# Performance work log

Hardware: AMD Instinct MI355X
Metric: run time of the kernel (lower is better)

Reference implementation:

```python
import jax, jax.numpy as jnp
import numpy as np

S, N, H = 2048, 32, 1024   # source len, batch, hidden_size
E = 1024                   # input_size (attention MLP width)


def setup_inputs() -> dict:
    key = jax.random.key(0)
    ks = jax.random.split(key, 8)
    sc_h = 1.0 / np.sqrt(H)
    sc_e = 1.0 / np.sqrt(E)
    return {
        "out_e": jax.random.normal(ks[0], (S, N, H), dtype=jnp.float32),
        "hidden_d": jax.random.normal(ks[1], (1, N, H), dtype=jnp.float32),
        "W1": jax.random.uniform(ks[2], (E, H), jnp.float32, -sc_h, sc_h),
        "b1": jax.random.uniform(ks[3], (E,), jnp.float32, -sc_h, sc_h),
        "W2": jax.random.uniform(ks[4], (E, H), jnp.float32, -sc_h, sc_h),
        "b2": jax.random.uniform(ks[5], (E,), jnp.float32, -sc_h, sc_h),
        "W3": jax.random.uniform(ks[6], (1, E), jnp.float32, -sc_e, sc_e),
        "b3": jax.random.uniform(ks[7], (1,), jnp.float32, -sc_e, sc_e),
    }


def reference(out_e, hidden_d, W1, b1, W2, b2, W3, b3):
    # hidden_d (1,N,H) broadcasts against out_e (S,N,H); no explicit repeat needed.
    h1 = jnp.einsum('one,he->onh'.replace('e', 'x'), hidden_d, W1.T) if False else None
    # linear1(hidden_d): (1,N,E); linear2(out_e): (S,N,E)
    proj = jnp.tanh(hidden_d @ W1.T + b1 + out_e @ W2.T + b2)      # (S,N,E)
    a = proj @ W3.T + b3                                           # (S,N,1)
    alpha = jax.nn.softmax(a, axis=0)                              # softmax over source dim S
    c = jnp.einsum('sne,snh->enh', alpha, out_e)                   # (1,N,H)
    return (c, alpha)
```

## Files before the change

kernel.cpp:

```cpp
#include <hip/hip_runtime.h>
#include <hip/hip_bf16.h>
#include <stdint.h>

constexpr int kS = 2048;
constexpr int kN = 32;
constexpr int kH = 1024;
constexpr int kE = 1024;
constexpr int kM = kS * kN;

constexpr int BM = 128;
constexpr int BE = 128;
constexpr int BK = 64;
constexpr int KSTEPS = kH / BK;

typedef __bf16 bf16x8 __attribute__((ext_vector_type(8)));
typedef float f32x4 __attribute__((ext_vector_type(4)));

__device__ __forceinline__ float tanh_fast(float x) {
    float e = __expf(2.0f * x);
    return 1.0f - 2.0f / (e + 1.0f);
}

__device__ __forceinline__ uint32_t f2bf_rne(float f) {
    uint32_t u = __builtin_bit_cast(uint32_t, f);
    u += 0x7FFFu + ((u >> 16) & 1u);
    return u >> 16;
}

__device__ __forceinline__ uint32_t pack2bf(float lo, float hi) {
    return f2bf_rne(lo) | (f2bf_rne(hi) << 16);
}

__global__ __launch_bounds__(64) void k1_h1c(const float* __restrict__ hd,
                                             const float* __restrict__ W1,
                                             const float* __restrict__ b1,
                                             const float* __restrict__ b2,
                                             float* __restrict__ h1c) {
    int e = blockIdx.x;
    int lane = threadIdx.x;
    const float4* wrow = (const float4*)(W1 + (size_t)e * kH);
    float4 w[4];
#pragma unroll
    for (int q = 0; q < 4; ++q) w[q] = wrow[lane + q * 64];
    float bb = b1[e] + b2[e];
    for (int n = 0; n < kN; ++n) {
        const float4* hrow = (const float4*)(hd + (size_t)n * kH);
        float p = 0.f;
#pragma unroll
        for (int q = 0; q < 4; ++q) {
            float4 h4 = hrow[lane + q * 64];
            p += w[q].x * h4.x + w[q].y * h4.y + w[q].z * h4.z + w[q].w * h4.w;
        }
#pragma unroll
        for (int o = 32; o; o >>= 1) p += __shfl_xor(p, o);
        if (lane == 0) h1c[n * kE + e] = p + bb;
    }
}

__global__ __launch_bounds__(256) void k2_cvt(const float* __restrict__ W2,
                                              unsigned short* __restrict__ W2b) {
    int i = blockIdx.x * 256 + threadIdx.x;
    float4 v = ((const float4*)W2)[i];
    uint2 o;
    o.x = pack2bf(v.x, v.y);
    o.y = pack2bf(v.z, v.w);
    ((uint2*)W2b)[i] = o;
}

__global__ __launch_bounds__(256, 2) void k3_gemm(const float* __restrict__ out_e,
                                                  const unsigned short* __restrict__ W2b,
                                                  const float* __restrict__ h1c,
                                                  const float* __restrict__ W3,
                                                  float* __restrict__ a_ws) {
    __shared__ __align__(16) unsigned short Abuf[2][BM * BK];
    __shared__ __align__(16) unsigned short Bbuf[2][BE * BK];

    const int tid = threadIdx.x;
    const int lane = tid & 63;
    const int w = tid >> 6;
    const int wr = w >> 1, wc = w & 1;
    const int l15 = lane & 15, lhi = lane >> 4;
    const int rowBase = (blockIdx.x >> 3) * BM;
    const int colBase = (blockIdx.x & 7) * BE;

    f32x4 acc[4][4];
#pragma unroll
    for (int m = 0; m < 4; ++m)
#pragma unroll
        for (int n = 0; n < 4; ++n)
#pragma unroll
            for (int j = 0; j < 4; ++j) {
                int rl = wr * 64 + m * 16 + lhi * 4 + j;
                int e = colBase + wc * 64 + n * 16 + l15;
                acc[m][n][j] = h1c[((rowBase + rl) & (kN - 1)) * kE + e];
            }

    auto stageA_load = [&](int ks, float4* regs) {
#pragma unroll
        for (int t = 0; t < 8; ++t) {
            int li = t * 256 + tid;
            int arow = li >> 4, akf = (li & 15) * 4;
            regs[t] = *(const float4*)(out_e + (size_t)(rowBase + arow) * kH + ks * BK + akf);
        }
    };
    auto stageB_load = [&](int ks, uint4* regs) {
#pragma unroll
        for (int t = 0; t < 4; ++t) {
            int li = t * 256 + tid;
            int brow = li >> 3, bk8 = (li & 7) * 8;
            regs[t] = *(const uint4*)(W2b + (size_t)(colBase + brow) * kH + ks * BK + bk8);
        }
    };
    auto stageA_write = [&](int buf, float4* regs) {
        char* base = (char*)Abuf[buf];
#pragma unroll
        for (int t = 0; t < 8; ++t) {
            int li = t * 256 + tid;
            int arow = li >> 4, akf = (li & 15) * 4;
            int off = arow * 128 + ((akf * 2) ^ ((arow & 7) << 4));
            uint2 val;
            val.x = pack2bf(regs[t].x, regs[t].y);
            val.y = pack2bf(regs[t].z, regs[t].w);
            *(uint2*)(base + off) = val;
        }
    };
    auto stageB_write = [&](int buf, uint4* regs) {
        char* base = (char*)Bbuf[buf];
#pragma unroll
        for (int t = 0; t < 4; ++t) {
            int li = t * 256 + tid;
            int brow = li >> 3, bk8 = (li & 7) * 8;
            int off = brow * 128 + ((bk8 * 2) ^ ((brow & 7) << 4));
            *(uint4*)(base + off) = regs[t];
        }
    };

    {
        float4 ar[8]; uint4 br[4];
        stageA_load(0, ar); stageB_load(0, br);
        stageA_write(0, ar); stageB_write(0, br);
    }
    __syncthreads();

    int cur = 0;
    for (int ks = 0; ks < KSTEPS; ++ks) {
        float4 ar[8]; uint4 br[4];
        if (ks + 1 < KSTEPS) { stageA_load(ks + 1, ar); stageB_load(ks + 1, br); }

        const char* Ab = (const char*)Abuf[cur];
        const char* Bb = (const char*)Bbuf[cur];
        bf16x8 af[2][4], bfr[2][4];
#pragma unroll
        for (int kk = 0; kk < 2; ++kk) {
            int kb = (kk * 32 + lhi * 8) * 2;
#pragma unroll
            for (int m = 0; m < 4; ++m) {
                int row = wr * 64 + m * 16 + l15;
                uint4 v = *(const uint4*)(Ab + row * 128 + (kb ^ ((row & 7) << 4)));
                af[kk][m] = __builtin_bit_cast(bf16x8, v);
            }
#pragma unroll
            for (int n = 0; n < 4; ++n) {
                int row = wc * 64 + n * 16 + l15;
                uint4 v = *(const uint4*)(Bb + row * 128 + (kb ^ ((row & 7) << 4)));
                bfr[kk][n] = __builtin_bit_cast(bf16x8, v);
            }
        }
#pragma unroll
        for (int kk = 0; kk < 2; ++kk)
#pragma unroll
            for (int m = 0; m < 4; ++m)
#pragma unroll
                for (int n = 0; n < 4; ++n)
                    acc[m][n] = __builtin_amdgcn_mfma_f32_16x16x32_bf16(af[kk][m], bfr[kk][n],
                                                                        acc[m][n], 0, 0, 0);
        __syncthreads();
        if (ks + 1 < KSTEPS) {
            stageA_write(cur ^ 1, ar);
            stageB_write(cur ^ 1, br);
            __syncthreads();
            cur ^= 1;
        }
    }

    float w3v[4];
#pragma unroll
    for (int n = 0; n < 4; ++n) w3v[n] = W3[colBase + wc * 64 + n * 16 + l15];
    float rs[4][4];
#pragma unroll
    for (int m = 0; m < 4; ++m)
#pragma unroll
        for (int j = 0; j < 4; ++j) {
            float v = 0.f;
#pragma unroll
            for (int n = 0; n < 4; ++n) v += w3v[n] * tanh_fast(acc[m][n][j]);
#pragma unroll
            for (int o = 1; o < 16; o <<= 1) v += __shfl_xor(v, o);
            rs[m][j] = v;
        }
    if (l15 == 0) {
#pragma unroll
        for (int m = 0; m < 4; ++m)
#pragma unroll
            for (int j = 0; j < 4; ++j)
                atomicAdd(&a_ws[rowBase + wr * 64 + m * 16 + lhi * 4 + j], rs[m][j]);
    }
}

__global__ __launch_bounds__(256) void k4_softmax(const float* __restrict__ a_ws,
                                                  float* __restrict__ alpha) {
    int n = blockIdx.x;
    int tid = threadIdx.x;
    __shared__ float red[4];
    float v[8];
    float mx = -1e30f;
#pragma unroll
    for (int i = 0; i < 8; ++i) {
        v[i] = a_ws[(i * 256 + tid) * kN + n];
        mx = fmaxf(mx, v[i]);
    }
#pragma unroll
    for (int o = 32; o; o >>= 1) mx = fmaxf(mx, __shfl_xor(mx, o));
    if ((tid & 63) == 0) red[tid >> 6] = mx;
    __syncthreads();
    mx = fmaxf(fmaxf(red[0], red[1]), fmaxf(red[2], red[3]));
    float sum = 0.f;
#pragma unroll
    for (int i = 0; i < 8; ++i) { v[i] = __expf(v[i] - mx); sum += v[i]; }
#pragma unroll
    for (int o = 32; o; o >>= 1) sum += __shfl_xor(sum, o);
    __syncthreads();
    if ((tid & 63) == 0) red[tid >> 6] = sum;
    __syncthreads();
    sum = red[0] + red[1] + red[2] + red[3];
    float inv = 1.0f / sum;
#pragma unroll
    for (int i = 0; i < 8; ++i) alpha[(i * 256 + tid) * kN + n] = v[i] * inv;
}

__global__ __launch_bounds__(256) void k5_part(const float* __restrict__ out_e,
                                               const float* __restrict__ alpha,
                                               float* __restrict__ c_part) {
    int n = blockIdx.x & 31;
    int sc = blockIdx.x >> 5;
    int tid = threadIdx.x;
    float4 acc = make_float4(0.f, 0.f, 0.f, 0.f);
    for (int s = sc * 128; s < sc * 128 + 128; ++s) {
        float al = alpha[s * kN + n];
        float4 x = *(const float4*)(out_e + ((size_t)s * kN + n) * kH + tid * 4);
        acc.x += al * x.x; acc.y += al * x.y; acc.z += al * x.z; acc.w += al * x.w;
    }
    *(float4*)(c_part + ((size_t)sc * kN + n) * kH + tid * 4) = acc;
}

__global__ __launch_bounds__(256) void k6_reduce(const float* __restrict__ c_part,
                                                 float* __restrict__ c) {
    int idx = blockIdx.x * 256 + threadIdx.x;
    float4 acc = make_float4(0.f, 0.f, 0.f, 0.f);
#pragma unroll
    for (int scn = 0; scn < 16; ++scn) {
        float4 x = ((const float4*)c_part)[scn * 8192 + idx];
        acc.x += x.x; acc.y += x.y; acc.z += x.z; acc.w += x.w;
    }
    ((float4*)c)[idx] = acc;
}

extern "C" void kernel_launch(void* const* d_in, const int* in_sizes, int n_in,
                              void* d_out, int out_size, void* d_ws, size_t ws_size,
                              hipStream_t stream) {
    const float* out_e = (const float*)d_in[0];
    const float* hidden_d = (const float*)d_in[1];
    const float* W1 = (const float*)d_in[2];
    const float* b1 = (const float*)d_in[3];
    const float* W2 = (const float*)d_in[4];
    const float* b2 = (const float*)d_in[5];
    const float* W3 = (const float*)d_in[6];

    float* out = (float*)d_out;
    float* c_out = out;
    float* alpha_out = out + kN * kH;

    char* ws = (char*)d_ws;
    unsigned short* W2b = (unsigned short*)ws;
    float* h1c = (float*)(ws + (2u << 20));
    float* a_ws = (float*)(ws + (2u << 20) + (128u << 10));
    float* c_part = (float*)(ws + (2u << 20) + (384u << 10));

    k1_h1c<<<kE, 64, 0, stream>>>(hidden_d, W1, b1, b2, h1c);
    k2_cvt<<<(kE * kH / 4) / 256, 256, 0, stream>>>(W2, W2b);
    (void)hipMemsetAsync(a_ws, 0, kM * sizeof(float), stream);
    k3_gemm<<<(kM / BM) * (kE / BE), 256, 0, stream>>>(out_e, W2b, h1c, W3, a_ws);
    k4_softmax<<<kN, 256, 0, stream>>>(a_ws, alpha_out);
    k5_part<<<16 * kN, 256, 0, stream>>>(out_e, alpha_out, c_part);
    k6_reduce<<<32, 256, 0, stream>>>(c_part, c_out);
}
```

Before: 704.1 us.

## Pre-convert out_e to bf16 and stream GEMM tiles via global_load_lds

Adds a pass that converts the whole out_e activation to bf16 in workspace, so the main GEMM can load A and B tiles straight into LDS with global_load_lds, skipping the register round trip and in-loop conversion. The swizzled LDS layout is kept by permuting 16-byte chunks per lane. This costs an extra full read of out_e (256MB fp32) plus a 128MB bf16 write, but cuts the GEMM's A-side traffic in half and frees VGPRs. It needs a large workspace and falls back to the old path when the workspace is too small.

```diff
diff --git a/kernel.cpp b/kernel.cpp
--- a/kernel.cpp
+++ b/kernel.cpp
@@ -29,6 +29,22 @@
 
 __device__ __forceinline__ uint32_t pack2bf(float lo, float hi) {
     return f2bf_rne(lo) | (f2bf_rne(hi) << 16);
+}
+
+__device__ __forceinline__ void gl_lds16(const void* g, void* l) {
+    __builtin_amdgcn_global_load_lds(
+        (const __attribute__((address_space(1))) uint32_t*)g,
+        (__attribute__((address_space(3))) uint32_t*)l, 16, 0, 0);
+}
+
+__global__ __launch_bounds__(256) void k0_cvtA(const float* __restrict__ in,
+                                               unsigned short* __restrict__ out) {
+    size_t i = (size_t)blockIdx.x * 256 + threadIdx.x;
+    float4 v = ((const float4*)in)[i];
+    uint2 o;
+    o.x = pack2bf(v.x, v.y);
+    o.y = pack2bf(v.z, v.w);
+    ((uint2*)out)[i] = o;
 }
 
 __global__ __launch_bounds__(64) void k1_h1c(const float* __restrict__ hd,
@@ -67,7 +83,9 @@
     ((uint2*)W2b)[i] = o;
 }
 
+template <bool DIRECT>
 __global__ __launch_bounds__(256, 2) void k3_gemm(const float* __restrict__ out_e,
+                                                  const unsigned short* __restrict__ Abf,
                                                   const unsigned short* __restrict__ W2b,
                                                   const float* __restrict__ h1c,
                                                   const float* __restrict__ W3,
@@ -94,6 +112,19 @@
                 int e = colBase + wc * 64 + n * 16 + l15;
                 acc[m][n][j] = h1c[((rowBase + rl) & (kN - 1)) * kE + e];
             }
+
+    const int r8 = lane >> 3;
+    const int schunk = (lane & 7) ^ r8;
+    auto stage_dma = [&](const unsigned short* src, int gRowBase, int ks, int buf,
+                         unsigned short(*ldsArr)[BM * BK]) {
+#pragma unroll
+        for (int i = 0; i < 4; ++i) {
+            int row = w * 32 + i * 8 + r8;
+            const void* g = src + (size_t)(gRowBase + row) * kH + ks * BK + schunk * 8;
+            void* l = (char*)ldsArr[buf] + w * 4096 + i * 1024;
+            gl_lds16(g, l);
+        }
+    };
 
     auto stageA_load = [&](int ks, float4* regs) {
 #pragma unroll
@@ -135,18 +166,7 @@
         }
     };
 
-    {
-        float4 ar[8]; uint4 br[4];
-        stageA_load(0, ar); stageB_load(0, br);
-        stageA_write(0, ar); stageB_write(0, br);
-    }
-    __syncthreads();
-
-    int cur = 0;
-    for (int ks = 0; ks < KSTEPS; ++ks) {
-        float4 ar[8]; uint4 br[4];
-        if (ks + 1 < KSTEPS) { stageA_load(ks + 1, ar); stageB_load(ks + 1, br); }
-
+    auto compute = [&](int cur) {
         const char* Ab = (const char*)Abuf[cur];
         const char* Bb = (const char*)Bbuf[cur];
         bf16x8 af[2][4], bfr[2][4];
@@ -174,12 +194,42 @@
                 for (int n = 0; n < 4; ++n)
                     acc[m][n] = __builtin_amdgcn_mfma_f32_16x16x32_bf16(af[kk][m], bfr[kk][n],
                                                                         acc[m][n], 0, 0, 0);
+    };
+
+    if (DIRECT) {
+        stage_dma(Abf, rowBase, 0, 0, Abuf);
+        stage_dma(W2b, colBase, 0, 0, Bbuf);
         __syncthreads();
-        if (ks + 1 < KSTEPS) {
-            stageA_write(cur ^ 1, ar);
-            stageB_write(cur ^ 1, br);
+        int cur = 0;
+#pragma unroll 4
+        for (int ks = 0; ks < KSTEPS; ++ks) {
+            if (ks + 1 < KSTEPS) {
+                stage_dma(Abf, rowBase, ks + 1, cur ^ 1, Abuf);
+                stage_dma(W2b, colBase, ks + 1, cur ^ 1, Bbuf);
+            }
+            compute(cur);
             __syncthreads();
             cur ^= 1;
+        }
+    } else {
+        {
+            float4 ar[8]; uint4 br[4];
+            stageA_load(0, ar); stageB_load(0, br);
+            stageA_write(0, ar); stageB_write(0, br);
+        }
+        __syncthreads();
+        int cur = 0;
+        for (int ks = 0; ks < KSTEPS; ++ks) {
+            float4 ar[8]; uint4 br[4];
+            if (ks + 1 < KSTEPS) { stageA_load(ks + 1, ar); stageB_load(ks + 1, br); }
+            compute(cur);
+            __syncthreads();
+            if (ks + 1 < KSTEPS) {
+                stageA_write(cur ^ 1, ar);
+                stageB_write(cur ^ 1, br);
+                __syncthreads();
+                cur ^= 1;
+            }
         }
     }
 
@@ -285,11 +335,18 @@
     float* h1c = (float*)(ws + (2u << 20));
     float* a_ws = (float*)(ws + (2u << 20) + (128u << 10));
     float* c_part = (float*)(ws + (2u << 20) + (384u << 10));
+    unsigned short* Abf = (unsigned short*)(ws + (5u << 20));
+    const size_t needed = (5ull << 20) + (size_t)kM * kH * 2;
+    const bool direct = ws_size >= needed;
 
     k1_h1c<<<kE, 64, 0, stream>>>(hidden_d, W1, b1, b2, h1c);
     k2_cvt<<<(kE * kH / 4) / 256, 256, 0, stream>>>(W2, W2b);
+    if (direct) k0_cvtA<<<(int)((size_t)kM * kH / 4 / 256), 256, 0, stream>>>(out_e, Abf);
     (void)hipMemsetAsync(a_ws, 0, kM * sizeof(float), stream);
-    k3_gemm<<<(kM / BM) * (kE / BE), 256, 0, stream>>>(out_e, W2b, h1c, W3, a_ws);
+    if (direct)
+        k3_gemm<true><<<(kM / BM) * (kE / BE), 256, 0, stream>>>(out_e, Abf, W2b, h1c, W3, a_ws);
+    else
+        k3_gemm<false><<<(kM / BM) * (kE / BE), 256, 0, stream>>>(out_e, Abf, W2b, h1c, W3, a_ws);
     k4_softmax<<<kN, 256, 0, stream>>>(a_ws, alpha_out);
     k5_part<<<16 * kN, 256, 0, stream>>>(out_e, alpha_out, c_part);
     k6_reduce<<<32, 256, 0, stream>>>(c_part, c_out);
```

Result: faster. 683.3 us (-2.9%).
